# Performance work log

Measured on AMD Instinct MI355X. Metric: run time of the kernel, lower is better.

## Reference

```python
import jax, jax.numpy as jnp
import numpy as np

B, H, Q, D = 8, 16, 256, 128
BLOCK_SIZE = 16
MAX_BLOCKS = 256          # blocks per sequence -> kv_len = 4096
NUM_BLOCKS = B * MAX_BLOCKS  # physical pool = 2048 blocks
NEG_INF = -1e9


def setup_inputs() -> dict:
    key = jax.random.key(0)
    k1, k2, k3, k4, k5 = jax.random.split(key, 5)
    q = jax.random.normal(k1, (B, H, Q, D), dtype=jnp.float32)
    k_cache = jax.random.normal(k2, (NUM_BLOCKS, H, BLOCK_SIZE, D), dtype=jnp.float32)
    v_cache = jax.random.normal(k3, (NUM_BLOCKS, H, BLOCK_SIZE, D), dtype=jnp.float32)
    # each sequence owns a disjoint, shuffled set of physical blocks (realistic paging)
    perm = jax.random.permutation(k4, NUM_BLOCKS)
    block_tables = perm.reshape(B, MAX_BLOCKS).astype(jnp.int32)
    # valid lengths in [2048, 4096] so softmax rows are never fully masked
    seq_lens = jax.random.randint(k5, (B,), 2048, MAX_BLOCKS * BLOCK_SIZE + 1).astype(jnp.int32)
    return {"q": q, "k_cache": k_cache, "v_cache": v_cache,
            "block_tables": block_tables, "seq_lens": seq_lens}


def paged_attention(q, k_cache, v_cache, block_tables, seq_lens):
    # Gather physical KV blocks per sequence via block tables.
    # k_cache: [N_blocks, H, bs, D]; block_tables: [B, M]
    k = k_cache[block_tables]                       # [B, M, H, bs, D]
    v = v_cache[block_tables]                       # [B, M, H, bs, D]
    kv_len = k.shape[1] * k.shape[3]
    k = jnp.transpose(k, (0, 2, 1, 3, 4)).reshape(q.shape[0], q.shape[1], kv_len, q.shape[3])
    v = jnp.transpose(v, (0, 2, 1, 3, 4)).reshape(q.shape[0], q.shape[1], kv_len, q.shape[3])
    scale = 1.0 / jnp.sqrt(jnp.asarray(q.shape[-1], q.dtype))
    scores = jnp.einsum('bhqd,bhkd->bhqk', q, k) * scale  # [B,H,Q,KV]
    pos = jnp.arange(kv_len)
    valid = pos[None, :] < seq_lens[:, None]               # [B, KV]
    scores = jnp.where(valid[:, None, None, :], scores, NEG_INF)
    attn = jax.nn.softmax(scores, axis=-1)
    return jnp.einsum('bhqk,bhkd->bhqd', attn, v)          # [B,H,Q,D]


def reference(q, k_cache, v_cache, block_tables, seq_lens):
    return paged_attention(q, k_cache, v_cache, block_tables, seq_lens)
```

## Files before the change

kernel.cpp:

```cpp
#include <hip/hip_runtime.h>
#include <hip/hip_bf16.h>

#define BB     8
#define HH     16
#define QLEN   256
#define DH     128
#define BSZ    16
#define MAXB   256
#define KT     64
#define BHQ    (BB*HH*QLEN)
#define VROW   144

typedef __attribute__((ext_vector_type(8)))  short bf16x8;
typedef __attribute__((ext_vector_type(16))) float f32x16;

__device__ __forceinline__ unsigned pk2(float a, float b) {
  union { __hip_bfloat162 h; unsigned u; } c;
  c.h = __float22bfloat162_rn(make_float2(a, b));
  return c.u;
}

__device__ __forceinline__ float bf2f(unsigned short u) {
  union { float f; unsigned u; } c; c.u = ((unsigned)u) << 16; return c.f;
}

__device__ __forceinline__ float fexp2(float x) {
#if __has_builtin(__builtin_amdgcn_exp2f)
  return __builtin_amdgcn_exp2f(x);
#else
  return exp2f(x);
#endif
}

__device__ __forceinline__ f32x16 mfma32(bf16x8 a, bf16x8 b, f32x16 c) {
  return __builtin_amdgcn_mfma_f32_32x32x16_bf16(a, b, c, 0, 0, 0);
}

__launch_bounds__(512, 2)
__global__ void paged_attn_kernel(const float* __restrict__ qg,
                                  const float* __restrict__ kc,
                                  const float* __restrict__ vc,
                                  const int* __restrict__ bt,
                                  const int* __restrict__ sl,
                                  float* __restrict__ outd,
                                  __hip_bfloat16* __restrict__ opart,
                                  float* __restrict__ mpart,
                                  float* __restrict__ lpart,
                                  int nkv) {
  __shared__ __align__(16) char kls[2][KT * DH * 2];
  __shared__ __align__(16) char vls[2][DH * VROW];
  __shared__ int btab[MAXB];

  const int tid  = threadIdx.x;
  const int wave = tid >> 6;
  const int lane = tid & 63;
  const int ll   = lane & 31;
  const int hi   = lane >> 5;

  const int bid = blockIdx.x;
  const int c   = bid % nkv;
  const int bh  = bid / nkv;
  const int b   = bh >> 4;
  const int h   = bh & 15;

  const int seq = sl[b];
  const int nt  = (seq + KT - 1) / KT;
  const int per = (nt + nkv - 1) / nkv;
  const int t0  = c * per;
  const int t1  = (t0 + per < nt) ? (t0 + per) : nt;

  if (tid < MAXB) btab[tid] = bt[b * MAXB + tid];
  __syncthreads();

  float4 kreg[2][2];
  float4 vreg[2][2];

#define ISSUE_LOADS(KV0)                                                        \
  {                                                                             \
    _Pragma("unroll")                                                           \
    for (int i = 0; i < 2; ++i) {                                               \
      const int slot = i * 512 + tid;                                           \
      const int row = slot >> 4, c16 = slot & 15;                               \
      const int kv = (KV0) + row;                                               \
      const int phys = btab[kv >> 4];                                           \
      const size_t gb = (((size_t)phys * HH + h) * BSZ + (kv & 15)) * DH + c16 * 8; \
      kreg[i][0] = *(const float4*)(kc + gb);                                   \
      kreg[i][1] = *(const float4*)(kc + gb + 4);                               \
    }                                                                           \
    _Pragma("unroll")                                                           \
    for (int i = 0; i < 2; ++i) {                                               \
      const int slot = i * 512 + tid;                                           \
      const int d4 = slot & 31, kvp = slot >> 5;                                \
      const int kv = (KV0) + kvp * 2;                                           \
      const int phys = btab[kv >> 4];                                           \
      const size_t gb = (((size_t)phys * HH + h) * BSZ + (kv & 15)) * DH + d4 * 4; \
      vreg[i][0] = *(const float4*)(vc + gb);                                   \
      vreg[i][1] = *(const float4*)(vc + gb + DH);                              \
    }                                                                           \
  }

  ISSUE_LOADS(t0 * KT)

  const float qscale = 0.08838834764831845f * 1.4426950408889634f;
  const int qbase = wave * 32;
  bf16x8 qf[8];
  {
    const float* qr = qg + ((size_t)bh * QLEN + qbase + ll) * DH;
#pragma unroll
    for (int ks = 0; ks < 8; ++ks) {
      const int d0 = ks * 16 + hi * 8;
      const float4 a  = *(const float4*)(qr + d0);
      const float4 bv = *(const float4*)(qr + d0 + 4);
      union { bf16x8 v; unsigned u[4]; } w;
      w.u[0] = pk2(a.x * qscale,  a.y * qscale);
      w.u[1] = pk2(a.z * qscale,  a.w * qscale);
      w.u[2] = pk2(bv.x * qscale, bv.y * qscale);
      w.u[3] = pk2(bv.z * qscale, bv.w * qscale);
      qf[ks] = w.v;
    }
  }

  f32x16 accT[4];
#pragma unroll
  for (int dt = 0; dt < 4; ++dt)
#pragma unroll
    for (int i = 0; i < 16; ++i) accT[dt][i] = 0.f;
  float mrow = -1e30f, lrow = 0.f;

  for (int t = t0; t < t1; ++t) {
    const int kv0 = t * KT;
    const int bb  = t & 1;

#pragma unroll
    for (int i = 0; i < 2; ++i) {
      const int slot = i * 512 + tid;
      const int row = slot >> 4, c16 = slot & 15;
      union { uint4 u4; unsigned u[4]; } w;
      w.u[0] = pk2(kreg[i][0].x, kreg[i][0].y);
      w.u[1] = pk2(kreg[i][0].z, kreg[i][0].w);
      w.u[2] = pk2(kreg[i][1].x, kreg[i][1].y);
      w.u[3] = pk2(kreg[i][1].z, kreg[i][1].w);
      const int kb = (row * 256 + c16 * 16) ^ ((row & 7) << 4);
      *(uint4*)(kls[bb] + kb) = w.u4;
    }
#pragma unroll
    for (int i = 0; i < 2; ++i) {
      const int slot = i * 512 + tid;
      const int d4 = slot & 31, kvp = slot >> 5;
      const float* aa = (const float*)&vreg[i][0];
      const float* bp = (const float*)&vreg[i][1];
#pragma unroll
      for (int jj = 0; jj < 4; ++jj) {
        const int d = d4 * 4 + jj;
        const int vb = d * VROW + ((kvp * 4) ^ (((d >> 3) & 7) << 4));
        *(unsigned*)(vls[bb] + vb) = pk2(aa[jj], bp[jj]);
      }
    }

    __syncthreads();

    if (t + 1 < t1) ISSUE_LOADS((t + 1) * KT)

    f32x16 s[2];
#pragma unroll
    for (int kvt = 0; kvt < 2; ++kvt) {
#pragma unroll
      for (int i = 0; i < 16; ++i) s[kvt][i] = 0.f;
      const int krow  = kvt * 32 + ll;
      const int kbase = krow * 256;
      const int ksw   = (krow & 7) << 4;
#pragma unroll
      for (int ks = 0; ks < 8; ++ks) {
        const bf16x8 kf = *(const bf16x8*)(kls[bb] + kbase + (((ks * 32 + hi * 16)) ^ ksw));
        s[kvt] = mfma32(kf, qf[ks], s[kvt]);
      }
    }

    if (kv0 + KT > seq) {
#pragma unroll
      for (int kvt = 0; kvt < 2; ++kvt)
#pragma unroll
        for (int r = 0; r < 16; ++r) {
          const int kvg = kv0 + kvt * 32 + (r & 3) + 8 * (r >> 2) + 4 * hi;
          if (kvg >= seq) s[kvt][r] = -1e30f;
        }
    }
    float tm[16];
#pragma unroll
    for (int r = 0; r < 16; ++r) tm[r] = fmaxf(s[0][r], s[1][r]);
#pragma unroll
    for (int w2 = 8; w2 >= 1; w2 >>= 1)
#pragma unroll
      for (int r = 0; r < w2; ++r) tm[r] = fmaxf(tm[r], tm[r + w2]);
    float mx = fmaxf(tm[0], __shfl_xor(tm[0], 32));
    if (!__all(mx - mrow <= 8.0f)) {
      const float mnew  = fmaxf(mrow, mx);
      const float alpha = fexp2(mrow - mnew);
      mrow = mnew;
      lrow *= alpha;
#pragma unroll
      for (int dt = 0; dt < 4; ++dt)
#pragma unroll
        for (int i = 0; i < 16; ++i) accT[dt][i] *= alpha;
    }
#pragma unroll
    for (int kvt = 0; kvt < 2; ++kvt)
#pragma unroll
      for (int r = 0; r < 16; ++r)
        s[kvt][r] = fexp2(s[kvt][r] - mrow);
    float ts[16];
#pragma unroll
    for (int r = 0; r < 16; ++r) ts[r] = s[0][r] + s[1][r];
#pragma unroll
    for (int w2 = 8; w2 >= 1; w2 >>= 1)
#pragma unroll
      for (int r = 0; r < w2; ++r) ts[r] += ts[r + w2];
    lrow += ts[0] + __shfl_xor(ts[0], 32);

    unsigned pkk[2][8];
#pragma unroll
    for (int kvt = 0; kvt < 2; ++kvt)
#pragma unroll
      for (int p = 0; p < 8; ++p)
        pkk[kvt][p] = pk2(s[kvt][2 * p], s[kvt][2 * p + 1]);

    bf16x8 pb[4];
#pragma unroll
    for (int kvb = 0; kvb < 4; ++kvb) {
      const int kvt = kvb >> 1;
      const int base = (kvb & 1) * 4;
      const unsigned send0 = hi ? pkk[kvt][base]     : pkk[kvt][base + 2];
      const unsigned send1 = hi ? pkk[kvt][base + 1] : pkk[kvt][base + 3];
      const unsigned recv0 = (unsigned)__shfl_xor((int)send0, 32);
      const unsigned recv1 = (unsigned)__shfl_xor((int)send1, 32);
      union { bf16x8 v; unsigned u[4]; } w;
      w.u[0] = hi ? recv0 : pkk[kvt][base];
      w.u[1] = hi ? recv1 : pkk[kvt][base + 1];
      w.u[2] = hi ? pkk[kvt][base + 2] : recv0;
      w.u[3] = hi ? pkk[kvt][base + 3] : recv1;
      pb[kvb] = w.v;
    }

#pragma unroll
    for (int dt = 0; dt < 4; ++dt) {
      const int d  = dt * 32 + ll;
      const int sw = ((d >> 3) & 7) << 4;
      const char* vbp = vls[bb] + d * VROW;
#pragma unroll
      for (int kvb = 0; kvb < 4; ++kvb) {
        const bf16x8 va = *(const bf16x8*)(vbp + ((kvb * 32 + hi * 16) ^ sw));
        accT[dt] = mfma32(va, pb[kvb], accT[dt]);
      }
    }
  }

  const int grow = bh * QLEN + qbase + ll;
  if (nkv == 1) {
    const float inv = 1.0f / lrow;
    float* orow = outd + (size_t)grow * DH;
#pragma unroll
    for (int dt = 0; dt < 4; ++dt)
#pragma unroll
      for (int r = 0; r < 4; ++r) {
        float4 v = make_float4(accT[dt][4 * r] * inv,     accT[dt][4 * r + 1] * inv,
                               accT[dt][4 * r + 2] * inv, accT[dt][4 * r + 3] * inv);
        *(float4*)(orow + dt * 32 + 8 * r + 4 * hi) = v;
      }
  } else {
    __hip_bfloat16* orow = opart + ((size_t)c * BHQ + grow) * DH;
#pragma unroll
    for (int dt = 0; dt < 4; ++dt)
#pragma unroll
      for (int r = 0; r < 4; ++r) {
        const unsigned lo2 = pk2(accT[dt][4 * r],     accT[dt][4 * r + 1]);
        const unsigned hi2 = pk2(accT[dt][4 * r + 2], accT[dt][4 * r + 3]);
        *(uint2*)((char*)orow + (dt * 32 + 8 * r + 4 * hi) * 2) = make_uint2(lo2, hi2);
      }
    if (hi == 0) {
      mpart[c * BHQ + grow] = mrow;
      lpart[c * BHQ + grow] = lrow;
    }
  }
}

__global__ void combine_kernel(const __hip_bfloat16* __restrict__ op,
                               const float* __restrict__ mp,
                               const float* __restrict__ lp,
                               float* __restrict__ out, int nkv) {
  const int idx = blockIdx.x * 256 + threadIdx.x;
  const int row = idx >> 4;
  float M = -1e30f;
  for (int cc = 0; cc < nkv; ++cc) M = fmaxf(M, mp[cc * BHQ + row]);
  float den = 0.f;
  float o[8] = {0.f, 0.f, 0.f, 0.f, 0.f, 0.f, 0.f, 0.f};
  for (int cc = 0; cc < nkv; ++cc) {
    const float w = exp2f(mp[cc * BHQ + row] - M);
    den += lp[cc * BHQ + row] * w;
    const uint4 v = *(const uint4*)((const char*)op + ((size_t)cc * BHQ * DH + (size_t)idx * 8) * 2);
    const unsigned u[4] = {v.x, v.y, v.z, v.w};
#pragma unroll
    for (int j = 0; j < 4; ++j) {
      o[2 * j]     += w * bf2f((unsigned short)(u[j] & 0xffffu));
      o[2 * j + 1] += w * bf2f((unsigned short)(u[j] >> 16));
    }
  }
  const float inv = 1.0f / den;
  float4* dst = (float4*)(out + (size_t)idx * 8);
  dst[0] = make_float4(o[0] * inv, o[1] * inv, o[2] * inv, o[3] * inv);
  dst[1] = make_float4(o[4] * inv, o[5] * inv, o[6] * inv, o[7] * inv);
}

extern "C" void kernel_launch(void* const* d_in, const int* in_sizes, int n_in,
                              void* d_out, int out_size, void* d_ws, size_t ws_size,
                              hipStream_t stream) {
  const float* q  = (const float*)d_in[0];
  const float* kc = (const float*)d_in[1];
  const float* vc = (const float*)d_in[2];
  const int* bt   = (const int*)d_in[3];
  const int* sl   = (const int*)d_in[4];
  float* out = (float*)d_out;

  const size_t perchunk = (size_t)BHQ * DH * sizeof(__hip_bfloat16) + (size_t)BHQ * 2 * sizeof(float);
  int nkv = 1;
  if (ws_size >= 4 * perchunk) nkv = 4;
  else if (ws_size >= 2 * perchunk) nkv = 2;

  __hip_bfloat16* op = (__hip_bfloat16*)d_ws;
  float* mp = (float*)((char*)d_ws + (size_t)nkv * BHQ * DH * sizeof(__hip_bfloat16));
  float* lp = mp + (size_t)nkv * BHQ;

  paged_attn_kernel<<<dim3(BB * HH * nkv), dim3(512), 0, stream>>>(q, kc, vc, bt, sl, out, op, mp, lp, nkv);
  if (nkv > 1)
    combine_kernel<<<dim3(BHQ * DH / 8 / 256), dim3(256), 0, stream>>>(op, mp, lp, out, nkv);
}
```

Measured before the change: 128.3 us.

## Restructure K/V double-buffer pipeline to prefetch two tiles ahead with chunk-major K layout

The LDS staging write for the next tile now happens right after the QK^T MFMAs of the current tile, and global loads are issued two tiles ahead. This moves the barrier to the end of the iteration so the wait on global memory overlaps more compute. The K tile in LDS is also reorganised from row-major with an XOR swizzle into 16-byte column chunks of 1KB, each with its own swizzle, to change the bank pattern of the MFMA operand reads. Register pressure rises because the next-next loads sit in registers while the current tile is computed, and the write into the alternate buffer depends on the single end-of-loop barrier for correctness.

```diff
diff --git a/kernel.cpp b/kernel.cpp
--- a/kernel.cpp
+++ b/kernel.cpp
@@ -47,7 +47,7 @@
                                   float* __restrict__ mpart,
                                   float* __restrict__ lpart,
                                   int nkv) {
-  __shared__ __align__(16) char kls[2][KT * DH * 2];
+  __shared__ __align__(16) char kls[2][16 * 1024];
   __shared__ __align__(16) char vls[2][DH * VROW];
   __shared__ int btab[MAXB];
 
@@ -99,6 +99,34 @@
     }                                                                           \
   }
 
+#define STAGE_WRITE(BUF)                                                        \
+  {                                                                             \
+    _Pragma("unroll")                                                           \
+    for (int i = 0; i < 2; ++i) {                                               \
+      const int slot = i * 512 + tid;                                           \
+      const int row = slot >> 4, c16 = slot & 15;                               \
+      union { uint4 u4; unsigned u[4]; } w;                                     \
+      w.u[0] = pk2(kreg[i][0].x, kreg[i][0].y);                                 \
+      w.u[1] = pk2(kreg[i][0].z, kreg[i][0].w);                                 \
+      w.u[2] = pk2(kreg[i][1].x, kreg[i][1].y);                                 \
+      w.u[3] = pk2(kreg[i][1].z, kreg[i][1].w);                                 \
+      *(uint4*)(kls[BUF] + c16 * 1024 + ((row ^ (c16 & 7)) << 4)) = w.u4;       \
+    }                                                                           \
+    _Pragma("unroll")                                                           \
+    for (int i = 0; i < 2; ++i) {                                               \
+      const int slot = i * 512 + tid;                                           \
+      const int d4 = slot & 31, kvp = slot >> 5;                                \
+      const float* aa = (const float*)&vreg[i][0];                              \
+      const float* bp = (const float*)&vreg[i][1];                              \
+      _Pragma("unroll")                                                         \
+      for (int jj = 0; jj < 4; ++jj) {                                          \
+        const int d = d4 * 4 + jj;                                              \
+        const int vb = d * VROW + ((kvp * 4) ^ (((d >> 3) & 7) << 4));          \
+        *(unsigned*)(vls[BUF] + vb) = pk2(aa[jj], bp[jj]);                      \
+      }                                                                         \
+    }                                                                           \
+  }
+
   ISSUE_LOADS(t0 * KT)
 
   const float qscale = 0.08838834764831845f * 1.4426950408889634f;
@@ -127,54 +155,29 @@
     for (int i = 0; i < 16; ++i) accT[dt][i] = 0.f;
   float mrow = -1e30f, lrow = 0.f;
 
+  STAGE_WRITE(t0 & 1)
+  if (t0 + 1 < t1) ISSUE_LOADS((t0 + 1) * KT)
+  __syncthreads();
+
   for (int t = t0; t < t1; ++t) {
     const int kv0 = t * KT;
     const int bb  = t & 1;
 
-#pragma unroll
-    for (int i = 0; i < 2; ++i) {
-      const int slot = i * 512 + tid;
-      const int row = slot >> 4, c16 = slot & 15;
-      union { uint4 u4; unsigned u[4]; } w;
-      w.u[0] = pk2(kreg[i][0].x, kreg[i][0].y);
-      w.u[1] = pk2(kreg[i][0].z, kreg[i][0].w);
-      w.u[2] = pk2(kreg[i][1].x, kreg[i][1].y);
-      w.u[3] = pk2(kreg[i][1].z, kreg[i][1].w);
-      const int kb = (row * 256 + c16 * 16) ^ ((row & 7) << 4);
-      *(uint4*)(kls[bb] + kb) = w.u4;
-    }
-#pragma unroll
-    for (int i = 0; i < 2; ++i) {
-      const int slot = i * 512 + tid;
-      const int d4 = slot & 31, kvp = slot >> 5;
-      const float* aa = (const float*)&vreg[i][0];
-      const float* bp = (const float*)&vreg[i][1];
-#pragma unroll
-      for (int jj = 0; jj < 4; ++jj) {
-        const int d = d4 * 4 + jj;
-        const int vb = d * VROW + ((kvp * 4) ^ (((d >> 3) & 7) << 4));
-        *(unsigned*)(vls[bb] + vb) = pk2(aa[jj], bp[jj]);
-      }
-    }
-
-    __syncthreads();
-
-    if (t + 1 < t1) ISSUE_LOADS((t + 1) * KT)
-
     f32x16 s[2];
 #pragma unroll
-    for (int kvt = 0; kvt < 2; ++kvt) {
-#pragma unroll
-      for (int i = 0; i < 16; ++i) s[kvt][i] = 0.f;
-      const int krow  = kvt * 32 + ll;
-      const int kbase = krow * 256;
-      const int ksw   = (krow & 7) << 4;
-#pragma unroll
-      for (int ks = 0; ks < 8; ++ks) {
-        const bf16x8 kf = *(const bf16x8*)(kls[bb] + kbase + (((ks * 32 + hi * 16)) ^ ksw));
-        s[kvt] = mfma32(kf, qf[ks], s[kvt]);
-      }
-    }
+    for (int i = 0; i < 16; ++i) { s[0][i] = 0.f; s[1][i] = 0.f; }
+#pragma unroll
+    for (int ks = 0; ks < 8; ++ks) {
+      const int cch = 2 * ks + hi;
+      const char* cb = kls[bb] + cch * 1024;
+      const bf16x8 kf0 = *(const bf16x8*)(cb + (((ll)      ^ (cch & 7)) << 4));
+      const bf16x8 kf1 = *(const bf16x8*)(cb + (((32 + ll) ^ (cch & 7)) << 4));
+      s[0] = mfma32(kf0, qf[ks], s[0]);
+      s[1] = mfma32(kf1, qf[ks], s[1]);
+    }
+
+    if (t + 1 < t1) STAGE_WRITE(bb ^ 1)
+    if (t + 2 < t1) ISSUE_LOADS((t + 2) * KT)
 
     if (kv0 + KT > seq) {
 #pragma unroll
@@ -252,6 +255,8 @@
         accT[dt] = mfma32(va, pb[kvb], accT[dt]);
       }
     }
+
+    __syncthreads();
   }
 
   const int grow = bh * QLEN + qbase + ll;
```

Measured after the change: 123.5 us. 3.7% less time.
